# Performance work log

Hardware: AMD Instinct MI355X
Metric: run time of the kernel (lower is better)

## Reference

```python
import jax, jax.numpy as jnp
import numpy as np

B, SEQ, DIM = 2, 2048, 1024
HEADS, DIM_HEAD = 16, 64
INNER = HEADS * DIM_HEAD
SCALE = DIM_HEAD ** -0.5


def rotate_half(x):
    # pair consecutive dims (d r) with r=2: (x1, x2) -> (-x2, x1)
    xp = x.reshape(*x.shape[:-1], -1, 2)
    x1, x2 = xp[..., 0], xp[..., 1]
    return jnp.stack((-x2, x1), axis=-1).reshape(x.shape)


def apply_rotary_emb(freqs, t):
    # freqs: [n, rot_dim] angles; t: [b, h, n, d]
    rot_dim = freqs.shape[-1]
    t_rot, t_pass = t[..., :rot_dim], t[..., rot_dim:]
    t_rot = t_rot * jnp.cos(freqs) + rotate_half(t_rot) * jnp.sin(freqs)
    return jnp.concatenate([t_rot, t_pass], axis=-1)


def setup_inputs() -> dict:
    key = jax.random.key(0)
    ks = jax.random.split(key, 4)
    x = jax.random.normal(ks[0], (B, SEQ, DIM), dtype=jnp.float32)
    mask = jnp.ones((B, SEQ), dtype=bool)
    rotary_pos_emb = jax.random.uniform(ks[1], (SEQ, DIM_HEAD), dtype=jnp.float32)
    Wqkv = jax.random.normal(ks[2], (DIM, 3 * INNER), dtype=jnp.float32) * 0.02
    Wout = jax.random.normal(ks[3], (INNER, DIM), dtype=jnp.float32) * 0.02
    bout = jnp.zeros((DIM,), dtype=jnp.float32)
    return {"x": x, "mask": mask, "rotary_pos_emb": rotary_pos_emb,
            "Wqkv": Wqkv, "Wout": Wout, "bout": bout}


def reference(x, mask, rotary_pos_emb, Wqkv, Wout, bout):
    b, n, _ = x.shape
    qkv = x @ Wqkv                                   # [b, n, 3*inner]
    q, k, v = jnp.split(qkv, 3, axis=-1)

    def to_heads(t):
        return t.reshape(b, n, HEADS, DIM_HEAD).transpose(0, 2, 1, 3)  # [b,h,n,d]

    q, k, v = to_heads(q), to_heads(k), to_heads(v)
    freqs = rotary_pos_emb[:n, :]
    # NB: original applies rotary to q, k AND v
    q = apply_rotary_emb(freqs, q)
    k = apply_rotary_emb(freqs, k)
    v = apply_rotary_emb(freqs, v)
    q = q * SCALE

    dots = jnp.einsum('bhid,bhjd->bhij', q, k)       # [b,h,n,n]
    mask_value = -jnp.finfo(dots.dtype).max
    pad = mask[:, None, None, :]                     # [b,1,1,n] keep where True
    dots = jnp.where(pad, dots, mask_value)
    idx = jnp.arange(n)
    causal = idx[None, :] > idx[:, None]             # j >= i + (j-i+1) with i==j==n
    dots = jnp.where(causal[None, None], mask_value, dots)

    attn = jax.nn.softmax(dots, axis=-1)
    out = jnp.einsum('bhij,bhjd->bhid', attn, v)     # [b,h,n,d]
    out = out.transpose(0, 2, 1, 3).reshape(b, n, INNER)
    return out @ Wout + bout
```

## Files before the change

### kernel.cpp

```cpp
#include <hip/hip_runtime.h>
#include <hip/hip_bf16.h>
#include <stdint.h>

#define DEVI __device__ __forceinline__

typedef __bf16 bf16x8 __attribute__((ext_vector_type(8)));
typedef float f32x4 __attribute__((ext_vector_type(4)));
typedef float f32x16 __attribute__((ext_vector_type(16)));

static constexpr int SEQ = 2048;
static constexpr int DIM = 1024;
static constexpr int HEADS = 16;
static constexpr int NQKV = 3072;
static constexpr int MROWS = 4096;
static constexpr float QSCALE = 0.125f;
static constexpr float LOG2E = 1.4426950408889634f;

DEVI unsigned short f2bf(float f) {
  unsigned int u = __builtin_bit_cast(unsigned int, f);
  u += 0x7FFFu + ((u >> 16) & 1u);
  return (unsigned short)(u >> 16);
}

DEVI bf16x8 ld8(const unsigned short* p) {
  return __builtin_bit_cast(bf16x8, *(const uint4*)p);
}

DEVI f32x4 mfma16(bf16x8 a, bf16x8 b, f32x4 c) {
  return __builtin_amdgcn_mfma_f32_16x16x32_bf16(a, b, c, 0, 0, 0);
}

DEVI f32x16 mfma32(bf16x8 a, bf16x8 b, f32x16 c) {
  return __builtin_amdgcn_mfma_f32_32x32x16_bf16(a, b, c, 0, 0, 0);
}

DEVI void load_lds16(const void* g, void* l) {
  __builtin_amdgcn_global_load_lds((const __attribute__((address_space(1))) void*)g,
                                   (__attribute__((address_space(3))) void*)l,
                                   16, 0, 0);
}

DEVI int swz(int row, int kelem) {
  return row * 64 + (kelem ^ ((row & 7) << 3));
}

DEVI unsigned cvtpk(float lo, float hi) {
  unsigned r;
  asm("v_cvt_pk_bf16_f32 %0, %1, %2" : "=v"(r) : "v"(lo), "v"(hi));
  return r;
}

DEVI void pl32swap(unsigned& a, unsigned& b) {
  asm volatile("v_permlane32_swap_b32 %0, %1" : "+v"(a), "+v"(b));
}
DEVI float xhalf_max(float v) { return fmaxf(v, __shfl_xor(v, 32)); }
DEVI float xhalf_sum(float v) { return v + __shfl_xor(v, 32); }

DEVI void transpose_tile(const float* __restrict__ in, unsigned short* __restrict__ out,
                         int Kd, int Nd, int bx, int by, int tid,
                         unsigned short (*T)[68]) {
  const int n0 = bx * 64, k0 = by * 64;
  const int rr = tid >> 4, cc = (tid & 15) * 4;
#pragma unroll
  for (int p = 0; p < 4; ++p) {
    const int r = p * 16 + rr;
    float4 f = *(const float4*)(in + (size_t)(k0 + r) * Nd + n0 + cc);
    T[r][cc + 0] = f2bf(f.x);
    T[r][cc + 1] = f2bf(f.y);
    T[r][cc + 2] = f2bf(f.z);
    T[r][cc + 3] = f2bf(f.w);
  }
  __syncthreads();
#pragma unroll
  for (int p = 0; p < 4; ++p) {
    const int rn = p * 16 + rr;
    ushort4 v;
    v.x = T[cc + 0][rn];
    v.y = T[cc + 1][rn];
    v.z = T[cc + 2][rn];
    v.w = T[cc + 3][rn];
    *(ushort4*)(out + (size_t)(n0 + rn) * Kd + k0 + cc) = v;
  }
}

__global__ __launch_bounds__(256) void k_prep(
    const float* __restrict__ x, unsigned short* __restrict__ xb,
    const float* __restrict__ rope, float* __restrict__ cosb, float* __restrict__ sinb,
    const float* __restrict__ Wqkv, unsigned short* __restrict__ wqkvt,
    const float* __restrict__ Wout, unsigned short* __restrict__ woutt) {
  __shared__ unsigned short T[64][68];
  const int bid = blockIdx.x, tid = threadIdx.x;
  if (bid < 4096) {
    const int i = bid * 256 + tid;
    float4 f = *(const float4*)(x + (size_t)i * 4);
    ushort4 v;
    v.x = f2bf(f.x); v.y = f2bf(f.y); v.z = f2bf(f.z); v.w = f2bf(f.w);
    *(ushort4*)(xb + (size_t)i * 4) = v;
  } else if (bid < 4608) {
    const int i = (bid - 4096) * 256 + tid;
    float f = rope[i];
    cosb[i] = cosf(f);
    sinb[i] = sinf(f);
  } else if (bid < 5376) {
    const int idx = bid - 4608;
    transpose_tile(Wqkv, wqkvt, DIM, NQKV, idx % 48, idx / 48, tid, T);
  } else {
    const int idx = bid - 5376;
    transpose_tile(Wout, woutt, DIM, DIM, idx % 16, idx / 16, tid, T);
  }
}

DEVI void gemm_mainloop64(const unsigned short* __restrict__ A,
                          const unsigned short* __restrict__ B, int K,
                          int m0, int n0,
                          unsigned short* As, unsigned short* Bs,
                          f32x4 (&acc)[4][4]) {
  const int lane = threadIdx.x & 63;
  const int wid = threadIdx.x >> 6;
  const int wm = wid >> 1, wn = wid & 1;
  const int rsub = lane >> 3;
  const int ksw = ((lane & 7) ^ rsub) * 8;
  for (int kt = 0; kt < K; kt += 64) {
    __syncthreads();
#pragma unroll
    for (int i = 0; i < 4; ++i) {
      const int chunk = wid * 4 + i;
      const int row = chunk * 8 + rsub;
      load_lds16(A + (size_t)(m0 + row) * K + kt + ksw, As + chunk * 512);
      load_lds16(B + (size_t)(n0 + row) * K + kt + ksw, Bs + chunk * 512);
    }
    __syncthreads();
#pragma unroll
    for (int kk = 0; kk < 2; ++kk) {
      bf16x8 af[4], bfv[4];
#pragma unroll
      for (int mi = 0; mi < 4; ++mi)
        af[mi] = ld8(&As[swz(wm * 64 + mi * 16 + (lane & 15),
                             kk * 32 + 8 * (lane >> 4))]);
#pragma unroll
      for (int ni = 0; ni < 4; ++ni)
        bfv[ni] = ld8(&Bs[swz(wn * 64 + ni * 16 + (lane & 15),
                              kk * 32 + 8 * (lane >> 4))]);
#pragma unroll
      for (int mi = 0; mi < 4; ++mi)
#pragma unroll
        for (int ni = 0; ni < 4; ++ni)
          acc[mi][ni] = mfma16(af[mi], bfv[ni], acc[mi][ni]);
    }
  }
}

__global__ __launch_bounds__(256) void k_gemm_qkv(
    const unsigned short* __restrict__ xb, const unsigned short* __restrict__ wt,
    const float* __restrict__ cosb, const float* __restrict__ sinb,
    unsigned short* __restrict__ qb, unsigned short* __restrict__ kb,
    unsigned short* __restrict__ vb) {
  __shared__ __align__(16) unsigned short As[128 * 64];
  __shared__ __align__(16) unsigned short Bs[128 * 64];
  const int m0 = blockIdx.x * 128, n0 = blockIdx.y * 128;
  f32x4 acc[4][4] = {};
  gemm_mainloop64(xb, wt, DIM, m0, n0, As, Bs, acc);
  const int lane = threadIdx.x & 63, wid = threadIdx.x >> 6;
  const int wm = wid >> 1, wn = wid & 1;
#pragma unroll
  for (int mi = 0; mi < 4; ++mi) {
#pragma unroll
    for (int ni = 0; ni < 4; ++ni) {
      const int ng = n0 + wn * 64 + ni * 16 + (lane & 15);
      const int d = ng & 63;
      const int part = ng >> 10;
      const int h = (ng & 1023) >> 6;
      const int mg0 = m0 + wm * 64 + mi * 16 + 4 * (lane >> 4);
      const int s0 = mg0 & (SEQ - 1), b = mg0 >> 11;
      const size_t bh = (size_t)(b * HEADS + h);
      if (part == 2) {
        ushort4 vv;
#pragma unroll
        for (int r = 0; r < 4; ++r) {
          const int s = s0 + r;
          float v = acc[mi][ni][r];
          float p = __shfl_xor(v, 1);
          float cv = cosb[(s << 6) + d], sv = sinb[(s << 6) + d];
          float rot = v * cv + ((d & 1) ? p : -p) * sv;
          ((unsigned short*)&vv)[r] = f2bf(rot);
        }
        *(ushort4*)(vb + (bh * 64 + d) * SEQ + s0) = vv;
      } else {
#pragma unroll
        for (int r = 0; r < 4; ++r) {
          const int s = s0 + r;
          float v = acc[mi][ni][r];
          float p = __shfl_xor(v, 1);
          float cv = cosb[(s << 6) + d], sv = sinb[(s << 6) + d];
          float rot = v * cv + ((d & 1) ? p : -p) * sv;
          if (part == 0) {
            qb[(bh * SEQ + s) * 64 + d] = f2bf(rot * (QSCALE * LOG2E));
          } else {
            kb[(bh * SEQ + s) * 64 + d] = f2bf(rot);
          }
        }
      }
    }
  }
}

__global__ __launch_bounds__(256) void k_flash(
    const unsigned short* __restrict__ qb, const unsigned short* __restrict__ kb,
    const unsigned short* __restrict__ vtb, unsigned short* __restrict__ ao) {
  __shared__ __align__(16) unsigned short Ks[2][2][64 * 64];
  __shared__ __align__(16) unsigned short Vt[2][2][64 * 64];
  const int bh = blockIdx.x;
  const int j = blockIdx.y;
  const int tid = threadIdx.x, lane = tid & 63, wid = tid >> 6;
  const int wq = wid >> 1, wk = wid & 1;
  const int la31 = lane & 31, h = lane >> 5;
  const unsigned short* kbh = kb + (size_t)bh * SEQ * 64;
  const unsigned short* vbh = vtb + (size_t)bh * 64 * SEQ;
  const int b = bh >> 4, hh = bh & 15;
  const int sslot = ((lane & 7) ^ (lane >> 3)) * 8;
  float* mrg = (float*)&Ks[0][0][0];
  const int mbase = wq * 2176;

  auto stage = [&](int buf, int t) {
    const int kv0 = t * 64;
#pragma unroll
    for (int i = 0; i < 4; ++i) {
      const int chunk = wq * 4 + i;
      const int row = chunk * 8 + (lane >> 3);
      load_lds16(kbh + ((size_t)(kv0 + row) << 6) + sslot, &Ks[buf][wk][chunk * 512]);
      load_lds16(vbh + (size_t)row * SEQ + kv0 + sslot, &Vt[buf][wk][chunk * 512]);
    }
  };

#pragma unroll 1
  for (int hf = 0; hf < 2; ++hf) {
    const int qt = hf == 0 ? (31 - j) : j;
    const int q0 = qt * 64 + wq * 32;
    const int qr = q0 + la31;
    const unsigned short* qp = qb + ((size_t)bh * SEQ + qr) * 64;
    bf16x8 qf0 = ld8(qp + 0 + 8 * h);
    bf16x8 qf1 = ld8(qp + 16 + 8 * h);
    bf16x8 qf2 = ld8(qp + 32 + 8 * h);
    bf16x8 qf3 = ld8(qp + 48 + 8 * h);

    f32x16 o0 = {}, o1 = {};
    float m = -1e30f, l = 0.f;
    const int nkv = qt + 1;
    const int nst = (nkv + 1) >> 1;

    if (wk < nkv) stage(0, wk);
#pragma unroll 1
    for (int st = 0; st < nst; ++st) {
      const int cur = st & 1;
      const int t = 2 * st + wk;
      __syncthreads();
      { const int tn = 2 * (st + 1) + wk; if (tn < nkv) stage(cur ^ 1, tn); }

      if (t < nkv) {
        const int kv0 = t * 64;
        const unsigned short* Kc = &Ks[cur][wk][0];
        const unsigned short* Vc = &Vt[cur][wk][0];
        f32x16 st0 = {}, st1 = {};
        __builtin_amdgcn_s_setprio(1);
#pragma unroll
        for (int ks = 0; ks < 4; ++ks) {
          bf16x8 qk = (ks == 0) ? qf0 : (ks == 1) ? qf1 : (ks == 2) ? qf2 : qf3;
          st0 = mfma32(ld8(&Kc[swz(la31, 16 * ks + 8 * h)]), qk, st0);
          st1 = mfma32(ld8(&Kc[swz(32 + la31, 16 * ks + 8 * h)]), qk, st1);
        }
        __builtin_amdgcn_s_setprio(0);
        if (kv0 + 63 > q0) {
#pragma unroll
          for (int r = 0; r < 16; ++r) {
            const int kvo = (r & 3) + 8 * (r >> 2) + 4 * h;
            st0[r] = (kv0 + kvo > qr) ? -1e30f : st0[r];
            st1[r] = (kv0 + 32 + kvo > qr) ? -1e30f : st1[r];
          }
        }
        float a8[8];
#pragma unroll
        for (int i = 0; i < 8; ++i)
          a8[i] = fmaxf(fmaxf(st0[i], st0[i + 8]), fmaxf(st1[i], st1[i + 8]));
        float a4_0 = fmaxf(a8[0], a8[4]), a4_1 = fmaxf(a8[1], a8[5]);
        float a4_2 = fmaxf(a8[2], a8[6]), a4_3 = fmaxf(a8[3], a8[7]);
        float pmax = fmaxf(fmaxf(a4_0, a4_1), fmaxf(a4_2, a4_3));
        const bool nor = __all(pmax <= m + 8.f);
        float scl = 1.f;
        if (!nor) {
          const float rowmax = xhalf_max(pmax);
          const float mnew = fmaxf(m, rowmax);
          scl = exp2f(m - mnew);
          m = mnew;
        }
#pragma unroll
        for (int r = 0; r < 16; ++r) {
          st0[r] = exp2f(st0[r] - m);
          st1[r] = exp2f(st1[r] - m);
        }
        float s8[8];
#pragma unroll
        for (int i = 0; i < 8; ++i)
          s8[i] = (st0[i] + st0[i + 8]) + (st1[i] + st1[i + 8]);
        float s4_0 = s8[0] + s8[4], s4_1 = s8[1] + s8[5];
        float s4_2 = s8[2] + s8[6], s4_3 = s8[3] + s8[7];
        float psum = (s4_0 + s4_1) + (s4_2 + s4_3);
        const float rowsum = xhalf_sum(psum);
        if (nor) {
          l += rowsum;
        } else {
          l = l * scl + rowsum;
#pragma unroll
          for (int r = 0; r < 16; ++r) { o0[r] *= scl; o1[r] *= scl; }
        }

        unsigned w0 = cvtpk(st0[0], st0[1]),   w1 = cvtpk(st0[2], st0[3]);
        unsigned w2 = cvtpk(st0[4], st0[5]),   w3 = cvtpk(st0[6], st0[7]);
        unsigned w4 = cvtpk(st0[8], st0[9]),   w5 = cvtpk(st0[10], st0[11]);
        unsigned w6 = cvtpk(st0[12], st0[13]), w7 = cvtpk(st0[14], st0[15]);
        pl32swap(w0, w2); pl32swap(w1, w3); pl32swap(w4, w6); pl32swap(w5, w7);
        const bf16x8 pa0 = __builtin_bit_cast(bf16x8, (uint4){w0, w1, w2, w3});
        const bf16x8 pa1 = __builtin_bit_cast(bf16x8, (uint4){w4, w5, w6, w7});
        unsigned x0 = cvtpk(st1[0], st1[1]),   x1 = cvtpk(st1[2], st1[3]);
        unsigned x2 = cvtpk(st1[4], st1[5]),   x3 = cvtpk(st1[6], st1[7]);
        unsigned x4 = cvtpk(st1[8], st1[9]),   x5 = cvtpk(st1[10], st1[11]);
        unsigned x6 = cvtpk(st1[12], st1[13]), x7 = cvtpk(st1[14], st1[15]);
        pl32swap(x0, x2); pl32swap(x1, x3); pl32swap(x4, x6); pl32swap(x5, x7);
        const bf16x8 pa2 = __builtin_bit_cast(bf16x8, (uint4){x0, x1, x2, x3});
        const bf16x8 pa3 = __builtin_bit_cast(bf16x8, (uint4){x4, x5, x6, x7});

        __builtin_amdgcn_s_setprio(1);
        o0 = mfma32(ld8(&Vc[swz(la31, 0 + 8 * h)]), pa0, o0);
        o0 = mfma32(ld8(&Vc[swz(la31, 16 + 8 * h)]), pa1, o0);
        o0 = mfma32(ld8(&Vc[swz(la31, 32 + 8 * h)]), pa2, o0);
        o0 = mfma32(ld8(&Vc[swz(la31, 48 + 8 * h)]), pa3, o0);
        o1 = mfma32(ld8(&Vc[swz(32 + la31, 0 + 8 * h)]), pa0, o1);
        o1 = mfma32(ld8(&Vc[swz(32 + la31, 16 + 8 * h)]), pa1, o1);
        o1 = mfma32(ld8(&Vc[swz(32 + la31, 32 + 8 * h)]), pa2, o1);
        o1 = mfma32(ld8(&Vc[swz(32 + la31, 48 + 8 * h)]), pa3, o1);
        __builtin_amdgcn_s_setprio(0);
      }
    }

    __syncthreads();
    if (wk == 1) {
#pragma unroll
      for (int s = 0; s < 8; ++s) {
        f32x4 c;
        if (s < 4) { c[0]=o0[4*s]; c[1]=o0[4*s+1]; c[2]=o0[4*s+2]; c[3]=o0[4*s+3]; }
        else       { c[0]=o1[4*(s-4)]; c[1]=o1[4*(s-4)+1]; c[2]=o1[4*(s-4)+2]; c[3]=o1[4*(s-4)+3]; }
        *(f32x4*)&mrg[mbase + lane * 32 + 4 * (s ^ (lane & 7))] = c;
      }
      mrg[mbase + 2048 + lane] = m;
      mrg[mbase + 2112 + lane] = l;
    }
    __syncthreads();
    if (wk == 0) {
      const float m1 = mrg[mbase + 2048 + lane];
      const float l1 = mrg[mbase + 2112 + lane];
      const float mM = fmaxf(m, m1);
      const float sc0 = exp2f(m - mM), sc1 = exp2f(m1 - mM);
      const float lt = l * sc0 + l1 * sc1;
      const float rl = __builtin_amdgcn_rcpf(lt);
      unsigned short* aor = ao + ((size_t)(b * SEQ + qr)) * 1024 + hh * 64;
#pragma unroll
      for (int s = 0; s < 8; ++s) {
        f32x4 c = *(const f32x4*)&mrg[mbase + lane * 32 + 4 * (s ^ (lane & 7))];
        float v0, v1, v2, v3;
        if (s < 4) {
          v0 = (o0[4*s]   * sc0 + c[0] * sc1) * rl;
          v1 = (o0[4*s+1] * sc0 + c[1] * sc1) * rl;
          v2 = (o0[4*s+2] * sc0 + c[2] * sc1) * rl;
          v3 = (o0[4*s+3] * sc0 + c[3] * sc1) * rl;
        } else {
          v0 = (o1[4*(s-4)]   * sc0 + c[0] * sc1) * rl;
          v1 = (o1[4*(s-4)+1] * sc0 + c[1] * sc1) * rl;
          v2 = (o1[4*(s-4)+2] * sc0 + c[2] * sc1) * rl;
          v3 = (o1[4*(s-4)+3] * sc0 + c[3] * sc1) * rl;
        }
        uint2 uv;
        uv.x = cvtpk(v0, v1);
        uv.y = cvtpk(v2, v3);
        *(uint2*)(aor + (s < 4 ? 8 * s : 32 + 8 * (s - 4)) + 4 * h) = uv;
      }
    }
    __syncthreads();
  }
}

__global__ __launch_bounds__(256) void k_gemm_out(
    const unsigned short* __restrict__ ao, const unsigned short* __restrict__ wt,
    const float* __restrict__ bout, float* __restrict__ out) {
  __shared__ __align__(16) unsigned short As[128 * 64];
  __shared__ __align__(16) unsigned short Bs[128 * 64];
  const int m0 = blockIdx.x * 128, n0 = blockIdx.y * 128;
  f32x4 acc[4][4] = {};
  gemm_mainloop64(ao, wt, DIM, m0, n0, As, Bs, acc);
  const int lane = threadIdx.x & 63, wid = threadIdx.x >> 6;
  const int wm = wid >> 1, wn = wid & 1;
#pragma unroll
  for (int mi = 0; mi < 4; ++mi) {
#pragma unroll
    for (int ni = 0; ni < 4; ++ni) {
      const int ng = n0 + wn * 64 + ni * 16 + (lane & 15);
      const float bn = bout[ng];
#pragma unroll
      for (int r = 0; r < 4; ++r) {
        const int mg = m0 + wm * 64 + mi * 16 + 4 * (lane >> 4) + r;
        out[(size_t)mg * DIM + ng] = acc[mi][ni][r] + bn;
      }
    }
  }
}

extern "C" void kernel_launch(void* const* d_in, const int* in_sizes, int n_in,
                              void* d_out, int out_size, void* d_ws, size_t ws_size,
                              hipStream_t stream) {
  const float* x    = (const float*)d_in[0];
  const float* rope = (const float*)d_in[2];
  const float* Wqkv = (const float*)d_in[3];
  const float* Wout = (const float*)d_in[4];
  const float* bout = (const float*)d_in[5];
  float* out = (float*)d_out;

  char* ws = (char*)d_ws;
  unsigned short* xb    = (unsigned short*)(ws + 0);
  unsigned short* wqkvt = (unsigned short*)(ws + 8388608);
  unsigned short* woutt = (unsigned short*)(ws + 14680064);
  float*          cosb  = (float*)(ws + 16777216);
  float*          sinb  = (float*)(ws + 17301504);
  unsigned short* qbuf  = (unsigned short*)(ws + 17825792);
  unsigned short* kbuf  = (unsigned short*)(ws + 26214400);
  unsigned short* vbuf  = (unsigned short*)(ws + 34603008);
  unsigned short* aob   = (unsigned short*)(ws + 42991616);

  k_prep<<<5632, 256, 0, stream>>>(x, xb, rope, cosb, sinb, Wqkv, wqkvt, Wout, woutt);
  k_gemm_qkv<<<dim3(MROWS / 128, NQKV / 128), 256, 0, stream>>>(xb, wqkvt, cosb, sinb,
                                                                qbuf, kbuf, vbuf);
  k_flash<<<dim3(32, 16), 256, 0, stream>>>(qbuf, kbuf, vbuf, aob);
  k_gemm_out<<<dim3(MROWS / 128, DIM / 128), 256, 0, stream>>>(aob, woutt, bout, out);
}
```

Measured before the change: 132.7 us.

## Split flash attention into one q-tile per block with 32-wide KV steps

Each flash-attention block now handles a single 64-row query tile instead of pairing a short and a long tile, and the grid doubles to 1024 blocks. Query tiles are assigned in an interleaved order to spread causal work across blocks. KV tiles shrink to 32 keys per warp per step, which halves the LDS footprint, trims the causal masking to only the diagonal tile, and gives finer-grained causal skipping. The cost is more loop iterations and barriers per unit of work, and less even per-block work than the paired scheme.

```diff
diff --git a/kernel.cpp b/kernel.cpp
--- a/kernel.cpp
+++ b/kernel.cpp
@@ -207,183 +207,168 @@
 __global__ __launch_bounds__(256) void k_flash(
     const unsigned short* __restrict__ qb, const unsigned short* __restrict__ kb,
     const unsigned short* __restrict__ vtb, unsigned short* __restrict__ ao) {
-  __shared__ __align__(16) unsigned short Ks[2][2][64 * 64];
-  __shared__ __align__(16) unsigned short Vt[2][2][64 * 64];
+  __shared__ __align__(16) unsigned short KV[2][2][2][2048];
   const int bh = blockIdx.x;
-  const int j = blockIdx.y;
+  const int jj = blockIdx.y;
+  const int j0 = jj & 7, jk = jj >> 3;
+  const int qt = (jk == 0) ? j0 : (jk == 1) ? 15 - j0
+               : (jk == 2) ? 16 + j0 : 31 - j0;
   const int tid = threadIdx.x, lane = tid & 63, wid = tid >> 6;
   const int wq = wid >> 1, wk = wid & 1;
   const int la31 = lane & 31, h = lane >> 5;
   const unsigned short* kbh = kb + (size_t)bh * SEQ * 64;
   const unsigned short* vbh = vtb + (size_t)bh * 64 * SEQ;
   const int b = bh >> 4, hh = bh & 15;
-  const int sslot = ((lane & 7) ^ (lane >> 3)) * 8;
-  float* mrg = (float*)&Ks[0][0][0];
+  float* mrg = (float*)&KV[0][0][0][0];
   const int mbase = wq * 2176;
 
+  const int pA = wq * 128 + lane;
+  const int pB = pA + 64;
+  const int rA = pA >> 3, rB = pB >> 3;
+  const int cA = (pA & 7) ^ (rA & 7), cB = (pB & 7) ^ (rB & 7);
+  const int kconA = rA * 64 + cA * 8, kconB = rB * 64 + cB * 8;
+  const int vconA = (2 * rA + (cA >> 2)) * SEQ + (cA & 3) * 8;
+  const int vconB = (2 * rB + (cB >> 2)) * SEQ + (cB & 3) * 8;
+
+  const int q0 = qt * 64 + wq * 32;
+  const int qr = q0 + la31;
+  const unsigned short* qp = qb + ((size_t)bh * SEQ + qr) * 64;
+  bf16x8 qf0 = ld8(qp + 0 + 8 * h);
+  bf16x8 qf1 = ld8(qp + 16 + 8 * h);
+  bf16x8 qf2 = ld8(qp + 32 + 8 * h);
+  bf16x8 qf3 = ld8(qp + 48 + 8 * h);
+
+  f32x16 o0 = {}, o1 = {};
+  float m = -1e30f, l = 0.f;
+  const int tmax = 2 * qt + wq;
+  const int tlim = 2 * qt + 1;
+
   auto stage = [&](int buf, int t) {
-    const int kv0 = t * 64;
-#pragma unroll
-    for (int i = 0; i < 4; ++i) {
-      const int chunk = wq * 4 + i;
-      const int row = chunk * 8 + (lane >> 3);
-      load_lds16(kbh + ((size_t)(kv0 + row) << 6) + sslot, &Ks[buf][wk][chunk * 512]);
-      load_lds16(vbh + (size_t)row * SEQ + kv0 + sslot, &Vt[buf][wk][chunk * 512]);
-    }
+    const size_t kv0 = (size_t)t * 32;
+    unsigned short* Kd = &KV[buf][wk][0][0];
+    unsigned short* Vd = &KV[buf][wk][1][0];
+    load_lds16(kbh + kv0 * 64 + kconA, Kd + pA * 8);
+    load_lds16(kbh + kv0 * 64 + kconB, Kd + pB * 8);
+    load_lds16(vbh + kv0 + vconA, Vd + pA * 8);
+    load_lds16(vbh + kv0 + vconB, Vd + pB * 8);
   };
 
+  stage(0, wk);
 #pragma unroll 1
-  for (int hf = 0; hf < 2; ++hf) {
-    const int qt = hf == 0 ? (31 - j) : j;
-    const int q0 = qt * 64 + wq * 32;
-    const int qr = q0 + la31;
-    const unsigned short* qp = qb + ((size_t)bh * SEQ + qr) * 64;
-    bf16x8 qf0 = ld8(qp + 0 + 8 * h);
-    bf16x8 qf1 = ld8(qp + 16 + 8 * h);
-    bf16x8 qf2 = ld8(qp + 32 + 8 * h);
-    bf16x8 qf3 = ld8(qp + 48 + 8 * h);
-
-    f32x16 o0 = {}, o1 = {};
-    float m = -1e30f, l = 0.f;
-    const int nkv = qt + 1;
-    const int nst = (nkv + 1) >> 1;
-
-    if (wk < nkv) stage(0, wk);
-#pragma unroll 1
-    for (int st = 0; st < nst; ++st) {
-      const int cur = st & 1;
-      const int t = 2 * st + wk;
-      __syncthreads();
-      { const int tn = 2 * (st + 1) + wk; if (tn < nkv) stage(cur ^ 1, tn); }
-
-      if (t < nkv) {
-        const int kv0 = t * 64;
-        const unsigned short* Kc = &Ks[cur][wk][0];
-        const unsigned short* Vc = &Vt[cur][wk][0];
-        f32x16 st0 = {}, st1 = {};
-        __builtin_amdgcn_s_setprio(1);
-#pragma unroll
-        for (int ks = 0; ks < 4; ++ks) {
-          bf16x8 qk = (ks == 0) ? qf0 : (ks == 1) ? qf1 : (ks == 2) ? qf2 : qf3;
-          st0 = mfma32(ld8(&Kc[swz(la31, 16 * ks + 8 * h)]), qk, st0);
-          st1 = mfma32(ld8(&Kc[swz(32 + la31, 16 * ks + 8 * h)]), qk, st1);
+  for (int stp = 0; stp <= qt; ++stp) {
+    const int buf = stp & 1;
+    const int t = 2 * stp + wk;
+    __syncthreads();
+    const int tn = t + 2;
+    if (tn <= tlim) stage(buf ^ 1, tn);
+
+    if (t <= tmax) {
+      const int kv0 = t * 32;
+      const unsigned short* Kc = &KV[buf][wk][0][0];
+      const unsigned short* Vc = &KV[buf][wk][1][0];
+      f32x16 st = {};
+      __builtin_amdgcn_s_setprio(1);
+      st = mfma32(ld8(&Kc[swz(la31, 0 + 8 * h)]), qf0, st);
+      st = mfma32(ld8(&Kc[swz(la31, 16 + 8 * h)]), qf1, st);
+      st = mfma32(ld8(&Kc[swz(la31, 32 + 8 * h)]), qf2, st);
+      st = mfma32(ld8(&Kc[swz(la31, 48 + 8 * h)]), qf3, st);
+      __builtin_amdgcn_s_setprio(0);
+      if (t == tmax && (wq == wk)) {
+#pragma unroll
+        for (int r = 0; r < 16; ++r) {
+          const int kvo = (r & 3) + 8 * (r >> 2) + 4 * h;
+          st[r] = (kv0 + kvo > qr) ? -1e30f : st[r];
         }
-        __builtin_amdgcn_s_setprio(0);
-        if (kv0 + 63 > q0) {
-#pragma unroll
-          for (int r = 0; r < 16; ++r) {
-            const int kvo = (r & 3) + 8 * (r >> 2) + 4 * h;
-            st0[r] = (kv0 + kvo > qr) ? -1e30f : st0[r];
-            st1[r] = (kv0 + 32 + kvo > qr) ? -1e30f : st1[r];
-          }
-        }
-        float a8[8];
-#pragma unroll
-        for (int i = 0; i < 8; ++i)
-          a8[i] = fmaxf(fmaxf(st0[i], st0[i + 8]), fmaxf(st1[i], st1[i + 8]));
-        float a4_0 = fmaxf(a8[0], a8[4]), a4_1 = fmaxf(a8[1], a8[5]);
-        float a4_2 = fmaxf(a8[2], a8[6]), a4_3 = fmaxf(a8[3], a8[7]);
-        float pmax = fmaxf(fmaxf(a4_0, a4_1), fmaxf(a4_2, a4_3));
-        const bool nor = __all(pmax <= m + 8.f);
-        float scl = 1.f;
-        if (!nor) {
-          const float rowmax = xhalf_max(pmax);
-          const float mnew = fmaxf(m, rowmax);
-          scl = exp2f(m - mnew);
-          m = mnew;
-        }
-#pragma unroll
-        for (int r = 0; r < 16; ++r) {
-          st0[r] = exp2f(st0[r] - m);
-          st1[r] = exp2f(st1[r] - m);
-        }
-        float s8[8];
-#pragma unroll
-        for (int i = 0; i < 8; ++i)
-          s8[i] = (st0[i] + st0[i + 8]) + (st1[i] + st1[i + 8]);
-        float s4_0 = s8[0] + s8[4], s4_1 = s8[1] + s8[5];
-        float s4_2 = s8[2] + s8[6], s4_3 = s8[3] + s8[7];
-        float psum = (s4_0 + s4_1) + (s4_2 + s4_3);
-        const float rowsum = xhalf_sum(psum);
-        if (nor) {
-          l += rowsum;
-        } else {
-          l = l * scl + rowsum;
-#pragma unroll
-          for (int r = 0; r < 16; ++r) { o0[r] *= scl; o1[r] *= scl; }
-        }
-
-        unsigned w0 = cvtpk(st0[0], st0[1]),   w1 = cvtpk(st0[2], st0[3]);
-        unsigned w2 = cvtpk(st0[4], st0[5]),   w3 = cvtpk(st0[6], st0[7]);
-        unsigned w4 = cvtpk(st0[8], st0[9]),   w5 = cvtpk(st0[10], st0[11]);
-        unsigned w6 = cvtpk(st0[12], st0[13]), w7 = cvtpk(st0[14], st0[15]);
-        pl32swap(w0, w2); pl32swap(w1, w3); pl32swap(w4, w6); pl32swap(w5, w7);
-        const bf16x8 pa0 = __builtin_bit_cast(bf16x8, (uint4){w0, w1, w2, w3});
-        const bf16x8 pa1 = __builtin_bit_cast(bf16x8, (uint4){w4, w5, w6, w7});
-        unsigned x0 = cvtpk(st1[0], st1[1]),   x1 = cvtpk(st1[2], st1[3]);
-        unsigned x2 = cvtpk(st1[4], st1[5]),   x3 = cvtpk(st1[6], st1[7]);
-        unsigned x4 = cvtpk(st1[8], st1[9]),   x5 = cvtpk(st1[10], st1[11]);
-        unsigned x6 = cvtpk(st1[12], st1[13]), x7 = cvtpk(st1[14], st1[15]);
-        pl32swap(x0, x2); pl32swap(x1, x3); pl32swap(x4, x6); pl32swap(x5, x7);
-        const bf16x8 pa2 = __builtin_bit_cast(bf16x8, (uint4){x0, x1, x2, x3});
-        const bf16x8 pa3 = __builtin_bit_cast(bf16x8, (uint4){x4, x5, x6, x7});
-
-        __builtin_amdgcn_s_setprio(1);
-        o0 = mfma32(ld8(&Vc[swz(la31, 0 + 8 * h)]), pa0, o0);
-        o0 = mfma32(ld8(&Vc[swz(la31, 16 + 8 * h)]), pa1, o0);
-        o0 = mfma32(ld8(&Vc[swz(la31, 32 + 8 * h)]), pa2, o0);
-        o0 = mfma32(ld8(&Vc[swz(la31, 48 + 8 * h)]), pa3, o0);
-        o1 = mfma32(ld8(&Vc[swz(32 + la31, 0 + 8 * h)]), pa0, o1);
-        o1 = mfma32(ld8(&Vc[swz(32 + la31, 16 + 8 * h)]), pa1, o1);
-        o1 = mfma32(ld8(&Vc[swz(32 + la31, 32 + 8 * h)]), pa2, o1);
-        o1 = mfma32(ld8(&Vc[swz(32 + la31, 48 + 8 * h)]), pa3, o1);
-        __builtin_amdgcn_s_setprio(0);
-      }
-    }
-
-    __syncthreads();
-    if (wk == 1) {
-#pragma unroll
-      for (int s = 0; s < 8; ++s) {
-        f32x4 c;
-        if (s < 4) { c[0]=o0[4*s]; c[1]=o0[4*s+1]; c[2]=o0[4*s+2]; c[3]=o0[4*s+3]; }
-        else       { c[0]=o1[4*(s-4)]; c[1]=o1[4*(s-4)+1]; c[2]=o1[4*(s-4)+2]; c[3]=o1[4*(s-4)+3]; }
-        *(f32x4*)&mrg[mbase + lane * 32 + 4 * (s ^ (lane & 7))] = c;
-      }
-      mrg[mbase + 2048 + lane] = m;
-      mrg[mbase + 2112 + lane] = l;
-    }
-    __syncthreads();
-    if (wk == 0) {
-      const float m1 = mrg[mbase + 2048 + lane];
-      const float l1 = mrg[mbase + 2112 + lane];
-      const float mM = fmaxf(m, m1);
-      const float sc0 = exp2f(m - mM), sc1 = exp2f(m1 - mM);
-      const float lt = l * sc0 + l1 * sc1;
-      const float rl = __builtin_amdgcn_rcpf(lt);
-      unsigned short* aor = ao + ((size_t)(b * SEQ + qr)) * 1024 + hh * 64;
-#pragma unroll
-      for (int s = 0; s < 8; ++s) {
-        f32x4 c = *(const f32x4*)&mrg[mbase + lane * 32 + 4 * (s ^ (lane & 7))];
-        float v0, v1, v2, v3;
-        if (s < 4) {
-          v0 = (o0[4*s]   * sc0 + c[0] * sc1) * rl;
-          v1 = (o0[4*s+1] * sc0 + c[1] * sc1) * rl;
-          v2 = (o0[4*s+2] * sc0 + c[2] * sc1) * rl;
-          v3 = (o0[4*s+3] * sc0 + c[3] * sc1) * rl;
-        } else {
-          v0 = (o1[4*(s-4)]   * sc0 + c[0] * sc1) * rl;
-          v1 = (o1[4*(s-4)+1] * sc0 + c[1] * sc1) * rl;
-          v2 = (o1[4*(s-4)+2] * sc0 + c[2] * sc1) * rl;
-          v3 = (o1[4*(s-4)+3] * sc0 + c[3] * sc1) * rl;
-        }
-        uint2 uv;
-        uv.x = cvtpk(v0, v1);
-        uv.y = cvtpk(v2, v3);
-        *(uint2*)(aor + (s < 4 ? 8 * s : 32 + 8 * (s - 4)) + 4 * h) = uv;
-      }
-    }
-    __syncthreads();
+      }
+      float a8[8];
+#pragma unroll
+      for (int i = 0; i < 8; ++i) a8[i] = fmaxf(st[i], st[i + 8]);
+      float a4_0 = fmaxf(a8[0], a8[4]), a4_1 = fmaxf(a8[1], a8[5]);
+      float a4_2 = fmaxf(a8[2], a8[6]), a4_3 = fmaxf(a8[3], a8[7]);
+      float pmax = fmaxf(fmaxf(a4_0, a4_1), fmaxf(a4_2, a4_3));
+      const bool nor = __all(pmax <= m + 8.f);
+      float scl = 1.f;
+      if (!nor) {
+        const float rowmax = xhalf_max(pmax);
+        const float mnew = fmaxf(m, rowmax);
+        scl = exp2f(m - mnew);
+        m = mnew;
+      }
+#pragma unroll
+      for (int r = 0; r < 16; ++r) st[r] = exp2f(st[r] - m);
+      float s8[8];
+#pragma unroll
+      for (int i = 0; i < 8; ++i) s8[i] = st[i] + st[i + 8];
+      float s4_0 = s8[0] + s8[4], s4_1 = s8[1] + s8[5];
+      float s4_2 = s8[2] + s8[6], s4_3 = s8[3] + s8[7];
+      float psum = (s4_0 + s4_1) + (s4_2 + s4_3);
+      const float rowsum = xhalf_sum(psum);
+      if (nor) {
+        l += rowsum;
+      } else {
+        l = l * scl + rowsum;
+#pragma unroll
+        for (int r = 0; r < 16; ++r) { o0[r] *= scl; o1[r] *= scl; }
+      }
+      unsigned w0 = cvtpk(st[0], st[1]),   w1 = cvtpk(st[2], st[3]);
+      unsigned w2 = cvtpk(st[4], st[5]),   w3 = cvtpk(st[6], st[7]);
+      unsigned w4 = cvtpk(st[8], st[9]),   w5 = cvtpk(st[10], st[11]);
+      unsigned w6 = cvtpk(st[12], st[13]), w7 = cvtpk(st[14], st[15]);
+      pl32swap(w0, w2); pl32swap(w1, w3); pl32swap(w4, w6); pl32swap(w5, w7);
+      const bf16x8 pa0 = __builtin_bit_cast(bf16x8, (uint4){w0, w1, w2, w3});
+      const bf16x8 pa1 = __builtin_bit_cast(bf16x8, (uint4){w4, w5, w6, w7});
+      const int rv = la31 >> 1;
+      const int cb = 32 * (la31 & 1) + 8 * h;
+      __builtin_amdgcn_s_setprio(1);
+      o0 = mfma32(ld8(&Vc[swz(rv, cb)]), pa0, o0);
+      o0 = mfma32(ld8(&Vc[swz(rv, cb + 16)]), pa1, o0);
+      o1 = mfma32(ld8(&Vc[swz(16 + rv, cb)]), pa0, o1);
+      o1 = mfma32(ld8(&Vc[swz(16 + rv, cb + 16)]), pa1, o1);
+      __builtin_amdgcn_s_setprio(0);
+    }
+  }
+
+  __syncthreads();
+  if (wk == 1) {
+#pragma unroll
+    for (int s = 0; s < 8; ++s) {
+      f32x4 c;
+      if (s < 4) { c[0]=o0[4*s]; c[1]=o0[4*s+1]; c[2]=o0[4*s+2]; c[3]=o0[4*s+3]; }
+      else       { c[0]=o1[4*(s-4)]; c[1]=o1[4*(s-4)+1]; c[2]=o1[4*(s-4)+2]; c[3]=o1[4*(s-4)+3]; }
+      *(f32x4*)&mrg[mbase + lane * 32 + 4 * (s ^ (lane & 7))] = c;
+    }
+    mrg[mbase + 2048 + lane] = m;
+    mrg[mbase + 2112 + lane] = l;
+  }
+  __syncthreads();
+  if (wk == 0) {
+    const float m1 = mrg[mbase + 2048 + lane];
+    const float l1 = mrg[mbase + 2112 + lane];
+    const float mM = fmaxf(m, m1);
+    const float sc0 = exp2f(m - mM), sc1 = exp2f(m1 - mM);
+    const float lt = l * sc0 + l1 * sc1;
+    const float rl = __builtin_amdgcn_rcpf(lt);
+    unsigned short* aor = ao + ((size_t)(b * SEQ + qr)) * 1024 + hh * 64;
+#pragma unroll
+    for (int s = 0; s < 8; ++s) {
+      f32x4 c = *(const f32x4*)&mrg[mbase + lane * 32 + 4 * (s ^ (lane & 7))];
+      float v0, v1, v2, v3;
+      if (s < 4) {
+        v0 = (o0[4*s]   * sc0 + c[0] * sc1) * rl;
+        v1 = (o0[4*s+1] * sc0 + c[1] * sc1) * rl;
+        v2 = (o0[4*s+2] * sc0 + c[2] * sc1) * rl;
+        v3 = (o0[4*s+3] * sc0 + c[3] * sc1) * rl;
+      } else {
+        v0 = (o1[4*(s-4)]   * sc0 + c[0] * sc1) * rl;
+        v1 = (o1[4*(s-4)+1] * sc0 + c[1] * sc1) * rl;
+        v2 = (o1[4*(s-4)+2] * sc0 + c[2] * sc1) * rl;
+        v3 = (o1[4*(s-4)+3] * sc0 + c[3] * sc1) * rl;
+      }
+      uint2 uv;
+      uv.x = cvtpk(v0, v1);
+      uv.y = cvtpk(v2, v3);
+      *(uint2*)(aor + (s < 4 ? 8 * s : 32 + 8 * (s - 4)) + 4 * h) = uv;
+    }
   }
 }
 
@@ -436,6 +421,6 @@
   k_prep<<<5632, 256, 0, stream>>>(x, xb, rope, cosb, sinb, Wqkv, wqkvt, Wout, woutt);
   k_gemm_qkv<<<dim3(MROWS / 128, NQKV / 128), 256, 0, stream>>>(xb, wqkvt, cosb, sinb,
                                                                 qbuf, kbuf, vbuf);
-  k_flash<<<dim3(32, 16), 256, 0, stream>>>(qbuf, kbuf, vbuf, aob);
+  k_flash<<<dim3(32, 32), 256, 0, stream>>>(qbuf, kbuf, vbuf, aob);
   k_gemm_out<<<dim3(MROWS / 128, DIM / 128), 256, 0, stream>>>(aob, woutt, bout, out);
 }
```

New measurement: 133.9 us. About the same (+0.9%).

## Rewrite QKV GEMM with 256x256 tiles, 8 waves, and pipelined LDS staging

Applied to the files above, without the earlier changes.

The QKV projection GEMM now runs 512-thread blocks over 256x256 output tiles, with each wave computing 128x64. Global-to-LDS loads are double-buffered and staggered across quarter-steps using explicit vmcnt waits and sched barriers, and MFMA sections are bracketed with setprio. The aim is more operand reuse per byte loaded and better overlap of memory traffic with matrix math. In exchange the grid shrinks to 192 blocks, which may underfill the CUs, and the larger per-thread accumulator raises register pressure.

```diff
diff --git a/kernel.cpp b/kernel.cpp
--- a/kernel.cpp
+++ b/kernel.cpp
@@ -150,27 +150,92 @@
   }
 }
 
-__global__ __launch_bounds__(256) void k_gemm_qkv(
+__global__ void k_gemm_qkv(
     const unsigned short* __restrict__ xb, const unsigned short* __restrict__ wt,
     const float* __restrict__ cosb, const float* __restrict__ sinb,
     unsigned short* __restrict__ qb, unsigned short* __restrict__ kb,
     unsigned short* __restrict__ vb) {
-  __shared__ __align__(16) unsigned short As[128 * 64];
-  __shared__ __align__(16) unsigned short Bs[128 * 64];
-  const int m0 = blockIdx.x * 128, n0 = blockIdx.y * 128;
-  f32x4 acc[4][4] = {};
-  gemm_mainloop64(xb, wt, DIM, m0, n0, As, Bs, acc);
-  const int lane = threadIdx.x & 63, wid = threadIdx.x >> 6;
-  const int wm = wid >> 1, wn = wid & 1;
-#pragma unroll
-  for (int mi = 0; mi < 4; ++mi) {
+  __shared__ __align__(16) unsigned short Ab[2][2][8192];
+  __shared__ __align__(16) unsigned short Bb[2][2][8192];
+  const int tid = threadIdx.x, lane = tid & 63, wid = tid >> 6;
+  const int wm = wid >> 2, wn = wid & 3;
+  const int m0 = blockIdx.x * 256, n0 = blockIdx.y * 256;
+  const int la15 = lane & 15, l16 = lane >> 4;
+  const int pS0 = tid, pS1 = tid + 512;
+  const int sr0 = pS0 >> 3, sr1 = pS1 >> 3;
+  const int sc0 = ((pS0 & 7) ^ (sr0 & 7)) * 8, sc1 = ((pS1 & 7) ^ (sr1 & 7)) * 8;
+
+  auto stageA = [&](int h, int s) {
+    const unsigned short* src = xb + (size_t)(m0 + h * 128) * DIM + s * 64;
+    unsigned short* dst = &Ab[s & 1][h][0];
+    load_lds16(src + (size_t)sr0 * DIM + sc0, dst + pS0 * 8);
+    load_lds16(src + (size_t)sr1 * DIM + sc1, dst + pS1 * 8);
+  };
+  auto stageB = [&](int h, int s) {
+    const unsigned short* src = wt + (size_t)(n0 + h * 128) * DIM + s * 64;
+    unsigned short* dst = &Bb[s & 1][h][0];
+    load_lds16(src + (size_t)sr0 * DIM + sc0, dst + pS0 * 8);
+    load_lds16(src + (size_t)sr1 * DIM + sc1, dst + pS1 * 8);
+  };
+
+  f32x4 acc[8][4] = {};
+  stageA(0, 0); stageA(1, 0); stageB(0, 0); stageB(1, 0);
+  stageA(0, 1); stageA(1, 1); stageB(0, 1); stageB(1, 1);
+
+#pragma unroll 1
+  for (int s = 0; s < 16; ++s) {
+    const unsigned short* Ah = &Ab[s & 1][wm][0];
+    const unsigned short* Bh = &Bb[s & 1][wn >> 1][0];
+    const int rb = (wn & 1) * 64;
+    bf16x8 bfr[4][2];
+#pragma unroll
+    for (int q = 0; q < 4; ++q) {
+      if (q == 0) {
+        if (s == 0) asm volatile("s_waitcnt vmcnt(8)" ::: "memory");
+        else        asm volatile("s_waitcnt vmcnt(4)" ::: "memory");
+        __syncthreads();
+      }
+      if (q == 2) __syncthreads();
+      bf16x8 afr[2][2];
+      if (q == 0) {
+#pragma unroll
+        for (int ni = 0; ni < 4; ++ni)
+#pragma unroll
+          for (int kk = 0; kk < 2; ++kk)
+            bfr[ni][kk] = ld8(&Bh[swz(rb + ni * 16 + la15, kk * 32 + 8 * l16)]);
+      }
+#pragma unroll
+      for (int mi = 0; mi < 2; ++mi)
+#pragma unroll
+        for (int kk = 0; kk < 2; ++kk)
+          afr[mi][kk] = ld8(&Ah[swz(q * 32 + mi * 16 + la15, kk * 32 + 8 * l16)]);
+      if (q == 0) { if (s >= 1 && s + 1 < 16) stageA(0, s + 1); }
+      else if (q == 1) { if (s >= 1 && s + 1 < 16) stageA(1, s + 1); }
+      else if (q == 2) { if (s + 2 < 16) stageB(0, s + 2); }
+      else             { if (s + 2 < 16) stageB(1, s + 2); }
+      asm volatile("s_waitcnt lgkmcnt(0)" ::: "memory");
+      __builtin_amdgcn_sched_barrier(0);
+      __builtin_amdgcn_s_setprio(1);
+#pragma unroll
+      for (int kk = 0; kk < 2; ++kk)
+#pragma unroll
+        for (int mi = 0; mi < 2; ++mi)
+#pragma unroll
+          for (int ni = 0; ni < 4; ++ni)
+            acc[2 * q + mi][ni] = mfma16(afr[mi][kk], bfr[ni][kk], acc[2 * q + mi][ni]);
+      __builtin_amdgcn_s_setprio(0);
+    }
+  }
+
+  const int part = n0 >> 10;
+#pragma unroll
+  for (int mq = 0; mq < 8; ++mq) {
 #pragma unroll
     for (int ni = 0; ni < 4; ++ni) {
-      const int ng = n0 + wn * 64 + ni * 16 + (lane & 15);
+      const int ng = n0 + wn * 64 + ni * 16 + la15;
       const int d = ng & 63;
-      const int part = ng >> 10;
       const int h = (ng & 1023) >> 6;
-      const int mg0 = m0 + wm * 64 + mi * 16 + 4 * (lane >> 4);
+      const int mg0 = m0 + wm * 128 + mq * 16 + 4 * l16;
       const int s0 = mg0 & (SEQ - 1), b = mg0 >> 11;
       const size_t bh = (size_t)(b * HEADS + h);
       if (part == 2) {
@@ -178,7 +243,7 @@
 #pragma unroll
         for (int r = 0; r < 4; ++r) {
           const int s = s0 + r;
-          float v = acc[mi][ni][r];
+          float v = acc[mq][ni][r];
           float p = __shfl_xor(v, 1);
           float cv = cosb[(s << 6) + d], sv = sinb[(s << 6) + d];
           float rot = v * cv + ((d & 1) ? p : -p) * sv;
@@ -189,7 +254,7 @@
 #pragma unroll
         for (int r = 0; r < 4; ++r) {
           const int s = s0 + r;
-          float v = acc[mi][ni][r];
+          float v = acc[mq][ni][r];
           float p = __shfl_xor(v, 1);
           float cv = cosb[(s << 6) + d], sv = sinb[(s << 6) + d];
           float rot = v * cv + ((d & 1) ? p : -p) * sv;
@@ -434,8 +499,8 @@
   unsigned short* aob   = (unsigned short*)(ws + 42991616);
 
   k_prep<<<5632, 256, 0, stream>>>(x, xb, rope, cosb, sinb, Wqkv, wqkvt, Wout, woutt);
-  k_gemm_qkv<<<dim3(MROWS / 128, NQKV / 128), 256, 0, stream>>>(xb, wqkvt, cosb, sinb,
-                                                                qbuf, kbuf, vbuf);
+  k_gemm_qkv<<<dim3(16, 12), 512, 0, stream>>>(xb, wqkvt, cosb, sinb,
+                                               qbuf, kbuf, vbuf);
   k_flash<<<dim3(32, 16), 256, 0, stream>>>(qbuf, kbuf, vbuf, aob);
   k_gemm_out<<<dim3(MROWS / 128, DIM / 128), 256, 0, stream>>>(aob, woutt, bout, out);
 }
```

Result: slower. 313.5 us (+136.3%).
